# Optimization experiments

Measured on AMD Instinct MI355X. Metric: run time of the kernel, lower is better.

## Reference

```python
import jax, jax.numpy as jnp
import numpy as np
from jax import lax

KERNEL = (2, 2)
STRIDE = (1, 1)

def setup_inputs() -> dict:
    key = jax.random.key(0)
    x = jax.random.normal(key, (16, 96, 224, 224), dtype=jnp.float32)
    return {"x": x}

def reference(x):
    # Valid max pooling over NCHW with window KERNEL, stride STRIDE.
    kR, kC = KERNEL
    sR, sC = STRIDE
    return lax.reduce_window(
        x,
        -jnp.inf,
        lax.max,
        window_dimensions=(1, 1, kR, kC),
        window_strides=(1, 1, sR, sC),
        padding="VALID",
    )
```

## Files before the change

kernel.cpp:

```cpp
#include <hip/hip_runtime.h>


#define W_IN    224
#define HW_IN   (224 * 224)
#define W_OUT   223
#define H_OUT   223
#define HW_OUT  (223 * 223)
#define CGROUPS 56
#define RSTRIPS 28

typedef float f4a __attribute__((ext_vector_type(4)));
typedef float f4u __attribute__((ext_vector_type(4), aligned(4)));

__global__ __launch_bounds__(256) void maxpool2x2_s1_strip8(
    const float* __restrict__ in, float* __restrict__ out) {
  int job = blockIdx.x * 256 + threadIdx.x;
  int cg  = job % CGROUPS;
  int t   = job / CGROUPS;
  int rs  = t % RSTRIPS;
  int nc  = t / RSTRIPS;

  int w  = cg * 4;
  int h0 = rs * 8;
  int nrows   = (rs == RSTRIPS - 1) ? 7 : 8;
  bool tailc  = (cg == CGROUPS - 1);

  const float* p = in  + (size_t)nc * HW_IN  + (size_t)h0 * W_IN  + w;
  float*       q = out + (size_t)nc * HW_OUT + (size_t)h0 * W_OUT + w;

  f4a a = *(const f4a*)p;
  float a4 = tailc ? a.w : p[4];

  #pragma unroll 4
  for (int r = 0; r < nrows; ++r) {
    p += W_IN;
    f4a b = *(const f4a*)p;
    float b4 = tailc ? b.w : p[4];

    float vx = fmaxf(a.x, b.x);
    float vy = fmaxf(a.y, b.y);
    float vz = fmaxf(a.z, b.z);
    float vw = fmaxf(a.w, b.w);
    float v4 = fmaxf(a4, b4);

    if (!tailc) {
      f4u o;
      o.x = fmaxf(vx, vy);
      o.y = fmaxf(vy, vz);
      o.z = fmaxf(vz, vw);
      o.w = fmaxf(vw, v4);
      *(f4u*)q = o;
    } else {
      q[0] = fmaxf(vx, vy);
      q[1] = fmaxf(vy, vz);
      q[2] = fmaxf(vz, vw);
    }
    q += W_OUT;

    a = b;
    a4 = b4;
  }
}

extern "C" void kernel_launch(void* const* d_in, const int* in_sizes, int n_in,
                              void* d_out, int out_size, void* d_ws, size_t ws_size,
                              hipStream_t stream) {
  const float* x = (const float*)d_in[0];
  float* out = (float*)d_out;
  const int jobs   = 16 * 96 * RSTRIPS * CGROUPS;
  const int blocks = jobs / 256;
  maxpool2x2_s1_strip8<<<blocks, 256, 0, stream>>>(x, out);
}
```

Baseline: 523.9 us.

## Use grid-stride loop with clamped overlapping tiles, upfront row loads, nontemporal stores

```diff
diff --git a/kernel.cpp b/kernel.cpp
--- a/kernel.cpp
+++ b/kernel.cpp
@@ -4,61 +4,54 @@
 #define W_IN    224
 #define HW_IN   (224 * 224)
 #define W_OUT   223
-#define H_OUT   223
 #define HW_OUT  (223 * 223)
 #define CGROUPS 56
 #define RSTRIPS 28
+#define JOBS    (16 * 96 * RSTRIPS * CGROUPS)
+#define NBLOCKS 2048
 
-typedef float f4a __attribute__((ext_vector_type(4)));
 typedef float f4u __attribute__((ext_vector_type(4), aligned(4)));
 
-__global__ __launch_bounds__(256) void maxpool2x2_s1_strip8(
+__global__ __launch_bounds__(256, 6) void maxpool2x2_s1_strip8u(
     const float* __restrict__ in, float* __restrict__ out) {
-  int job = blockIdx.x * 256 + threadIdx.x;
-  int cg  = job % CGROUPS;
-  int t   = job / CGROUPS;
-  int rs  = t % RSTRIPS;
-  int nc  = t / RSTRIPS;
+  const int stride = NBLOCKS * 256;
+  for (int job = blockIdx.x * 256 + threadIdx.x; job < JOBS; job += stride) {
+    int cg = job % CGROUPS;
+    int t  = job / CGROUPS;
+    int rs = t % RSTRIPS;
+    int nc = t / RSTRIPS;
 
-  int w  = cg * 4;
-  int h0 = rs * 8;
-  int nrows   = (rs == RSTRIPS - 1) ? 7 : 8;
-  bool tailc  = (cg == CGROUPS - 1);
+    int w  = cg * 4;  if (w > 219) w = 219;
+    int h0 = rs * 8;  if (h0 > 215) h0 = 215;
 
-  const float* p = in  + (size_t)nc * HW_IN  + (size_t)h0 * W_IN  + w;
-  float*       q = out + (size_t)nc * HW_OUT + (size_t)h0 * W_OUT + w;
+    const float* p = in  + (size_t)nc * HW_IN  + (size_t)h0 * W_IN  + w;
+    float*       q = out + (size_t)nc * HW_OUT + (size_t)h0 * W_OUT + w;
 
-  f4a a = *(const f4a*)p;
-  float a4 = tailc ? a.w : p[4];
+    f4u   row[9];
+    float e[9];
+    #pragma unroll
+    for (int r = 0; r < 9; ++r) {
+      const float* pr = p + r * W_IN;
+      row[r] = *(const f4u*)pr;
+      e[r]   = pr[4];
+    }
 
-  #pragma unroll 4
-  for (int r = 0; r < nrows; ++r) {
-    p += W_IN;
-    f4a b = *(const f4a*)p;
-    float b4 = tailc ? b.w : p[4];
+    #pragma unroll
+    for (int r = 0; r < 8; ++r) {
+      f4u a = row[r], b = row[r + 1];
+      float vx = fmaxf(a.x, b.x);
+      float vy = fmaxf(a.y, b.y);
+      float vz = fmaxf(a.z, b.z);
+      float vw = fmaxf(a.w, b.w);
+      float v4 = fmaxf(e[r], e[r + 1]);
 
-    float vx = fmaxf(a.x, b.x);
-    float vy = fmaxf(a.y, b.y);
-    float vz = fmaxf(a.z, b.z);
-    float vw = fmaxf(a.w, b.w);
-    float v4 = fmaxf(a4, b4);
-
-    if (!tailc) {
       f4u o;
       o.x = fmaxf(vx, vy);
       o.y = fmaxf(vy, vz);
       o.z = fmaxf(vz, vw);
       o.w = fmaxf(vw, v4);
-      *(f4u*)q = o;
-    } else {
-      q[0] = fmaxf(vx, vy);
-      q[1] = fmaxf(vy, vz);
-      q[2] = fmaxf(vz, vw);
+      __builtin_nontemporal_store(o, (f4u*)(q + (size_t)r * W_OUT));
     }
-    q += W_OUT;
-
-    a = b;
-    a4 = b4;
   }
 }
 
@@ -67,7 +60,8 @@
                               hipStream_t stream) {
   const float* x = (const float*)d_in[0];
   float* out = (float*)d_out;
-  const int jobs   = 16 * 96 * RSTRIPS * CGROUPS;
-  const int blocks = jobs / 256;
-  maxpool2x2_s1_strip8<<<blocks, 256, 0, stream>>>(x, out);
+  int blocks = NBLOCKS;
+  int maxb = (JOBS + 255) / 256;
+  if (blocks > maxb) blocks = maxb;
+  maxpool2x2_s1_strip8u<<<blocks, 256, 0, stream>>>(x, out);
 }
```

New measurement: 532.1 us. Within noise of the previous version (+1.6%).
